# Kernel optimization log

Hardware: AMD Instinct MI355X
Metric: run time of the kernel (lower is better)

The kernel has to match this reference:

```python
import jax, jax.numpy as jnp
import numpy as np

MAX_LEN = 2048
D_MODEL = 1024
NUM_HEADS = 16
D_HEAD = D_MODEL // NUM_HEADS
BATCH = 2
SEQ = 2048


def setup_inputs() -> dict:
    key = jax.random.key(0)
    ks = jax.random.split(key, 8)
    scale = 1.0 / np.sqrt(D_MODEL)
    return {
        "x": jax.random.normal(ks[0], (BATCH, SEQ, D_MODEL), dtype=jnp.float32),
        "Wq": jax.random.normal(ks[1], (D_MODEL, D_MODEL), dtype=jnp.float32) * scale,
        "bq": jnp.zeros((D_MODEL,), dtype=jnp.float32),
        "Wk": jax.random.normal(ks[2], (D_MODEL, D_MODEL), dtype=jnp.float32) * scale,
        "bk": jnp.zeros((D_MODEL,), dtype=jnp.float32),
        "Wv": jax.random.normal(ks[3], (D_MODEL, D_MODEL), dtype=jnp.float32) * scale,
        "bv": jnp.zeros((D_MODEL,), dtype=jnp.float32),
        "Er": jax.random.normal(ks[4], (MAX_LEN, D_HEAD), dtype=jnp.float32),
    }


def _skew(QEr):
    # QEr: [B, H, S, S] -> Transformer-XL skew -> Srel: [B, H, S, S]
    B, H, S, _ = QEr.shape
    padded = jnp.pad(QEr, ((0, 0), (0, 0), (0, 0), (1, 0)))  # [B,H,S,S+1]
    reshaped = padded.reshape(B, H, S + 1, S)
    return reshaped[:, :, 1:, :]


def reference(x, Wq, bq, Wk, bk, Wv, bv, Er):
    B, S, D = x.shape
    H, dh = NUM_HEADS, D // NUM_HEADS
    q = (x @ Wq + bq).reshape(B, S, H, dh).transpose(0, 2, 1, 3)  # [B,H,S,dh]
    k = (x @ Wk + bk).reshape(B, S, H, dh).transpose(0, 2, 1, 3)
    v = (x @ Wv + bv).reshape(B, S, H, dh).transpose(0, 2, 1, 3)
    Er_s = Er[MAX_LEN - S:, :]                                    # [S, dh]
    QEr = jnp.einsum("bhsd,ld->bhsl", q, Er_s)                    # [B,H,S,S]
    Srel = _skew(QEr)
    QKt = jnp.einsum("bhsd,bhtd->bhst", q, k)
    attn = (QKt + Srel) / jnp.sqrt(jnp.asarray(dh, x.dtype))
    causal = jnp.tril(jnp.ones((S, S), dtype=bool))
    attn = jnp.where(causal[None, None], attn, -jnp.inf)
    attn = jax.nn.softmax(attn, axis=-1)
    out = jnp.einsum("bhst,bhtd->bhsd", attn, v)                  # [B,H,S,dh]
    return out.transpose(0, 2, 1, 3).reshape(B, S, D)             # dropout in eval = identity
```

## Files before the change

### kernel.cpp

```cpp
#include <hip/hip_runtime.h>
#include <hip/hip_bf16.h>

#define SLEN   2048
#define DMODEL 1024
#define NHEADS 16
#define DHEAD  64
#define NBATCH 2
#define EPAD_ROWS 2432

#define QSCALE 0.18033688011112042f
#define EXPB   23.083120654223414f

typedef __bf16 bf16x8 __attribute__((ext_vector_type(8)));
typedef float  f32x4  __attribute__((ext_vector_type(4)));

__device__ __forceinline__ unsigned short f2bf(float f) {
    unsigned int u = __builtin_bit_cast(unsigned int, f);
    return (unsigned short)((u + 0x7fffu + ((u >> 16) & 1u)) >> 16);
}

__device__ __forceinline__ float exp2_hw(float x) {
    float r;
    asm("v_exp_f32 %0, %1" : "=v"(r) : "v"(x));
    return r;
}

__device__ __forceinline__ unsigned int cvtpk_bf16(float lo, float hi) {
    unsigned int d;
    asm("v_cvt_pk_bf16_f32 %0, %1, %2" : "=v"(d) : "v"(lo), "v"(hi));
    return d;
}

__device__ __forceinline__ bf16x8 ld8(const unsigned short* p) {
    union { uint4 u; bf16x8 b; } t;
    t.u = *(const uint4*)p;
    return t.b;
}

__device__ __forceinline__ void glds16(const unsigned short* g, unsigned short* l) {
    __builtin_amdgcn_global_load_lds(
        (const __attribute__((address_space(1))) unsigned int*)g,
        (__attribute__((address_space(3))) unsigned int*)l, 16, 0, 0);
}

__global__ __launch_bounds__(256) void prep_kernel(
    const float* __restrict__ x, const float* __restrict__ Er,
    const float* __restrict__ Wq, const float* __restrict__ Wk,
    const float* __restrict__ Wv,
    unsigned short* __restrict__ xb, unsigned short* __restrict__ Ep,
    unsigned short* __restrict__ Wt) {
    const int bi = blockIdx.x, tid = threadIdx.x;
    if (bi < 4096) {
        int i = (bi * 256 + tid) * 4;
        float4 v = *(const float4*)(x + i);
        ushort4 o;
        o.x = f2bf(v.x); o.y = f2bf(v.y); o.z = f2bf(v.z); o.w = f2bf(v.w);
        *(ushort4*)(xb + i) = o;
    } else if (bi < 4704) {
        int i = (bi - 4096) * 256 + tid;
        int row = i >> 6;
        unsigned short v = 0;
        if (row < SLEN) v = f2bf(Er[i]);
        Ep[i] = v;
    } else {
        __shared__ float tile[32][33];
        const int b3 = bi - 4704;
        const int z = b3 >> 10, rem = b3 & 1023;
        const int n0 = (rem & 31) * 32, k0 = (rem >> 5) * 32;
        const float* W = (z == 0) ? Wq : (z == 1 ? Wk : Wv);
        unsigned short* out = Wt + (size_t)z * DMODEL * DMODEL;
        const int tx = tid & 31, ty = tid >> 5;
        for (int r = 0; r < 32; r += 8)
            tile[ty + r][tx] = W[(size_t)(k0 + ty + r) * DMODEL + n0 + tx];
        __syncthreads();
        for (int r = 0; r < 32; r += 8)
            out[(size_t)(n0 + ty + r) * DMODEL + k0 + tx] = f2bf(tile[tx][ty + r]);
    }
}

__global__ __launch_bounds__(256, 3) void qkv_gemm(
    const unsigned short* __restrict__ xb, const unsigned short* __restrict__ Wt,
    const float* __restrict__ bq, const float* __restrict__ bk, const float* __restrict__ bv,
    unsigned short* __restrict__ Qs, unsigned short* __restrict__ Ks,
    unsigned short* __restrict__ Vts) {
    const int b = blockIdx.x;
    const int x7 = b & 7, s = b >> 3;
    const int mt = ((x7 >> 1) << 3) | (s & 7);
    const int ntile = ((x7 & 1) << 2) | ((s >> 3) & 3);
    const int z = s >> 5;
    const int m0 = mt * 128, n0 = ntile * 128;

    const float* bias = (z == 0) ? bq : (z == 1 ? bk : bv);
    const unsigned short* Wz = Wt + (size_t)z * DMODEL * DMODEL;

    __shared__ __align__(16) unsigned short As[128][64];
    __shared__ __align__(16) unsigned short Bs[128][64];

    const int tid = threadIdx.x;
    const int wave = tid >> 6, lane = tid & 63, l16 = lane & 15, quad = lane >> 4;
    const int wm = (wave >> 1) * 64, wn = (wave & 1) * 64;

    const int lr8 = lane >> 3;
    const int sc  = ((lane & 7) ^ lr8) * 8;

    f32x4 acc[4][4];
#pragma unroll
    for (int mi = 0; mi < 4; mi++)
#pragma unroll
        for (int ni = 0; ni < 4; ni++) acc[mi][ni] = (f32x4){0.f, 0.f, 0.f, 0.f};

    for (int j = 0; j < 16; ++j) {
        if (j) __syncthreads();
        const int k0 = j * 64;
#pragma unroll
        for (int c = 0; c < 4; c++) {
            const int seg = wave * 4 + c;
            const int r8  = seg * 8 + lr8;
            glds16(&xb[(size_t)(m0 + r8) * DMODEL + k0 + sc], &As[seg * 8][0]);
            glds16(&Wz[(size_t)(n0 + r8) * DMODEL + k0 + sc], &Bs[seg * 8][0]);
        }
        __syncthreads();

        const unsigned short (*Aarr)[64] = (z == 2) ? Bs : As;
        const unsigned short (*Barr)[64] = (z == 2) ? As : Bs;
#pragma unroll
        for (int ks = 0; ks < 2; ks++) {
            const int pc = ((ks * 4 + quad) ^ (l16 & 7)) * 8;
            bf16x8 a[4], bb[4];
#pragma unroll
            for (int mi = 0; mi < 4; mi++) a[mi] = ld8(&Aarr[wm + mi * 16 + l16][pc]);
#pragma unroll
            for (int ni = 0; ni < 4; ni++) bb[ni] = ld8(&Barr[wn + ni * 16 + l16][pc]);
#pragma unroll
            for (int mi = 0; mi < 4; mi++)
#pragma unroll
                for (int ni = 0; ni < 4; ni++)
                    acc[mi][ni] = __builtin_amdgcn_mfma_f32_16x16x32_bf16(a[mi], bb[ni], acc[mi][ni], 0, 0, 0);
        }
    }

    if (z == 2) {
#pragma unroll
        for (int mi = 0; mi < 4; mi++)
#pragma unroll
            for (int r = 0; r < 4; r++) {
                const int n = n0 + wm + mi * 16 + quad * 4 + r;
                const float bb = bias[n];
                const int h = n >> 6, d = n & 63;
#pragma unroll
                for (int ni = 0; ni < 4; ni++) {
                    const int m = m0 + wn + ni * 16 + l16;
                    const int bi = m >> 11, ss = m & 2047;
                    Vts[((size_t)((bi * NHEADS + h) * 64 + d)) * SLEN + ss] = f2bf(acc[mi][ni][r] + bb);
                }
            }
    } else {
#pragma unroll
        for (int ni = 0; ni < 4; ni++) {
            const int n = n0 + wn + ni * 16 + l16;
            const float bb = bias[n];
            const int h = n >> 6, d = n & 63;
#pragma unroll
            for (int mi = 0; mi < 4; mi++)
#pragma unroll
                for (int r = 0; r < 4; r++) {
                    const int m = m0 + wm + mi * 16 + quad * 4 + r;
                    const int bi = m >> 11, ss = m & 2047;
                    float v = acc[mi][ni][r] + bb;
                    if (z == 0)
                        Qs[((size_t)(bi * NHEADS + h) * SLEN + ss) * 64 + d] = f2bf(v * QSCALE);
                    else
                        Ks[((size_t)(bi * NHEADS + h) * SLEN + ss) * 64 + d] = f2bf(v);
                }
        }
    }
}

__global__ __launch_bounds__(256, 2) void attn_kernel(
    const unsigned short* __restrict__ Q,
    const unsigned short* __restrict__ K,
    const unsigned short* __restrict__ Vt,
    const unsigned short* __restrict__ Ep,
    float* __restrict__ out) {
    const int tid = threadIdx.x;
    const int wave = tid >> 6, lane = tid & 63, l16 = lane & 15, quad = lane >> 4;
    const int lr8 = lane >> 3;
    const int swz = ((lane & 7) ^ lr8) * 8;

    const int bh = blockIdx.x & 31;
    const int pg = blockIdx.x >> 5;

    __shared__ __align__(16) unsigned short Ksh[2][64 * 64];
    __shared__ __align__(16) unsigned short Vsh[2][64 * 64];
    __shared__ __align__(16) unsigned short Esh[256 * 64];

    const unsigned short* Qb = Q + (size_t)bh * SLEN * 64;
    const unsigned short* Kb = K + (size_t)bh * SLEN * 64;
    const unsigned short* Vb = Vt + (size_t)bh * 64 * SLEN;
    const int ob = bh >> 4, oh = bh & 15;

    const int pc0 = (quad ^ (l16 & 7)) * 8;
    const int pc1 = ((4 + quad) ^ (l16 & 7)) * 8;
    const int krot = (15 - l16) & 3;
    const bool c1 = (krot & 1) != 0, c2 = (krot & 2) != 0;
    int permE[4]; bool hiE[4];
#pragma unroll
    for (int r = 0; r < 4; r++) {
        const int idx = quad * 4 + r + 15 - l16;
        permE[r] = ((idx >> 2) & 3) * 16 + l16;
        const int c  = r + 15 - l16;
        const int qv = (quad - (c >> 2)) & 3;
        hiE[r] = (qv * 4 + c) >= 16;
    }

    int s0 = pg * 64;
    int ntp = pg + 1;

#pragma unroll 1
    for (int pass = 0; pass < 2; ++pass) {
        const int sw = s0 + 16 * wave;
        const bf16x8 aq0 = ld8(Qb + (size_t)(sw + l16) * 64 + quad * 8);
        const bf16x8 aq1 = ld8(Qb + (size_t)(sw + l16) * 64 + 32 + quad * 8);

        f32x4 accO[4];
        float sacc[4];
#pragma unroll
        for (int nt = 0; nt < 4; nt++) accO[nt] = (f32x4){0.f, 0.f, 0.f, 0.f};
#pragma unroll
        for (int r = 0; r < 4; r++) sacc[r] = 0.f;

        const int p0row = SLEN - 64 - s0;

#pragma unroll
        for (int c = 0; c < 2; c++) {
            const int seg = wave * 2 + c;
            glds16(&Kb[(size_t)(seg * 8 + lr8) * 64 + swz], &Ksh[0][seg * 8 * 64]);
            glds16(&Vb[(size_t)(seg * 8 + lr8) * SLEN + swz], &Vsh[0][seg * 8 * 64]);
        }
#pragma unroll
        for (int u = 0; u < 6; u++) {
            const int idx = wave * 6 + u;
            const int grow = p0row + idx * 8;
            glds16(&Ep[(size_t)(grow + lr8) * 64 + swz], &Esh[(grow & 255) * 64]);
        }
        __syncthreads();

        for (int j = 0; j < ntp; ++j) {
            const int t0 = j * 64;
            const int cur = j & 1;

            if (j + 1 < ntp) {
                const int t1 = t0 + 64, nb = cur ^ 1;
#pragma unroll
                for (int c = 0; c < 2; c++) {
                    const int seg = wave * 2 + c;
                    glds16(&Kb[(size_t)(t1 + seg * 8 + lr8) * 64 + swz], &Ksh[nb][seg * 8 * 64]);
                    glds16(&Vb[(size_t)(seg * 8 + lr8) * SLEN + t1 + swz], &Vsh[nb][seg * 8 * 64]);
                }
                const int er = p0row + t0 + 128;
#pragma unroll
                for (int c = 0; c < 2; c++) {
                    const int seg = wave * 2 + c;
                    glds16(&Ep[(size_t)(er + seg * 8 + lr8) * 64 + swz],
                           &Esh[((er + seg * 8) & 255) * 64]);
                }
            }

            f32x4 accS[4];
#pragma unroll
            for (int nt = 0; nt < 4; nt++)
                accS[nt] = (f32x4){-EXPB, -EXPB, -EXPB, -EXPB};
#pragma unroll
            for (int nt = 0; nt < 4; nt++) {
                bf16x8 bk0 = ld8(&Ksh[cur][(nt * 16 + l16) * 64 + pc0]);
                bf16x8 bk1 = ld8(&Ksh[cur][(nt * 16 + l16) * 64 + pc1]);
                accS[nt] = __builtin_amdgcn_mfma_f32_16x16x32_bf16(bk0, aq0, accS[nt], 0, 0, 0);
                accS[nt] = __builtin_amdgcn_mfma_f32_16x16x32_bf16(bk1, aq1, accS[nt], 0, 0, 0);
            }

            const int rm0 = (SLEN - 16 - sw + t0) & 255;
            f32x4 accE[5];
#pragma unroll
            for (int nt = 0; nt < 5; nt++) accE[nt] = (f32x4){0.f, 0.f, 0.f, 0.f};
#pragma unroll
            for (int nt = 0; nt < 5; nt++) {
                const int rowm = (rm0 + nt * 16 + l16) & 255;
                bf16x8 be0 = ld8(&Esh[rowm * 64 + pc0]);
                bf16x8 be1 = ld8(&Esh[rowm * 64 + pc1]);
                accE[nt] = __builtin_amdgcn_mfma_f32_16x16x32_bf16(be0, aq0, accE[nt], 0, 0, 0);
                accE[nt] = __builtin_amdgcn_mfma_f32_16x16x32_bf16(be1, aq1, accE[nt], 0, 0, 0);
            }

            f32x4 rotE[5];
#pragma unroll
            for (int g = 0; g < 5; g++) {
                f32x4 A = accE[g], t, rt;
#pragma unroll
                for (int r = 0; r < 4; r++) t[r] = c1 ? A[(r + 1) & 3] : A[r];
#pragma unroll
                for (int r = 0; r < 4; r++) rt[r] = c2 ? t[(r + 2) & 3] : t[r];
                rotE[g] = rt;
            }

            float pe[4][4];
            auto scoreblk = [&](bool masked) {
#pragma unroll
                for (int nt = 0; nt < 4; nt++) {
#pragma unroll
                    for (int r = 0; r < 4; r++) {
                        float send = hiE[r] ? rotE[nt + 1][r] : rotE[nt][r];
                        float rel = __shfl(send, permE[r]);
                        float p = exp2_hw(accS[nt][r] + rel);
                        if (masked)
                            p = (t0 + nt * 16 + quad * 4 + r <= sw + l16) ? p : 0.0f;
                        sacc[r] += p;
                        pe[nt][r] = p;
                    }
                }
            };
            if (t0 + 63 <= sw) scoreblk(false);
            else               scoreblk(true);

            unsigned int w[4][2];
#pragma unroll
            for (int nt = 0; nt < 4; nt++) {
                w[nt][0] = cvtpk_bf16(pe[nt][0], pe[nt][1]);
                w[nt][1] = cvtpk_bf16(pe[nt][2], pe[nt][3]);
            }
            bf16x8 pf[2];
#pragma unroll
            for (int c = 0; c < 2; c++) {
                unsigned int a0 = w[2 * c][0], b0 = w[2 * c + 1][0];
                unsigned int a1 = w[2 * c][1], b1 = w[2 * c + 1][1];
                asm volatile("v_permlane32_swap_b32 %0, %1" : "+v"(a0), "+v"(b0));
                asm volatile("v_permlane16_swap_b32 %0, %1" : "+v"(a0), "+v"(b0));
                asm volatile("v_permlane32_swap_b32 %0, %1" : "+v"(a1), "+v"(b1));
                asm volatile("v_permlane16_swap_b32 %0, %1" : "+v"(a1), "+v"(b1));
                union { uint4 u; bf16x8 b; } t;
                t.u = (uint4){a0, a1, b0, b1};
                pf[c] = t.b;
            }

#pragma unroll
            for (int ntd = 0; ntd < 4; ntd++) {
                bf16x8 bv0 = ld8(&Vsh[cur][(ntd * 16 + l16) * 64 + pc0]);
                bf16x8 bv1 = ld8(&Vsh[cur][(ntd * 16 + l16) * 64 + pc1]);
                accO[ntd] = __builtin_amdgcn_mfma_f32_16x16x32_bf16(bv0, pf[0], accO[ntd], 0, 0, 0);
                accO[ntd] = __builtin_amdgcn_mfma_f32_16x16x32_bf16(bv1, pf[1], accO[ntd], 0, 0, 0);
            }

            __syncthreads();
        }

        float s4 = (sacc[0] + sacc[1]) + (sacc[2] + sacc[3]);
        s4 += __shfl_xor(s4, 16);
        s4 += __shfl_xor(s4, 32);
        const float inv = 1.f / s4;
        const int srow = sw + l16;
        float* orow = out + ((size_t)(ob * SLEN + srow)) * DMODEL + oh * 64 + quad * 4;
#pragma unroll
        for (int ntd = 0; ntd < 4; ntd++) {
            float4 st = {accO[ntd][0] * inv, accO[ntd][1] * inv,
                         accO[ntd][2] * inv, accO[ntd][3] * inv};
            *(float4*)(orow + ntd * 16) = st;
        }

        s0 = (31 - pg) * 64;
        ntp = 32 - pg;
    }
}

extern "C" void kernel_launch(void* const* d_in, const int* in_sizes, int n_in,
                              void* d_out, int out_size, void* d_ws, size_t ws_size,
                              hipStream_t stream) {
    const float* x  = (const float*)d_in[0];
    const float* Wq = (const float*)d_in[1];
    const float* bq = (const float*)d_in[2];
    const float* Wk = (const float*)d_in[3];
    const float* bk = (const float*)d_in[4];
    const float* Wv = (const float*)d_in[5];
    const float* bv = (const float*)d_in[6];
    const float* Er = (const float*)d_in[7];
    float* out = (float*)d_out;

    char* p = (char*)d_ws;
    unsigned short* xb  = (unsigned short*)p; p += (size_t)4096 * 1024 * 2;
    unsigned short* Wt  = (unsigned short*)p; p += (size_t)3 * 1024 * 1024 * 2;
    unsigned short* Qs  = (unsigned short*)p; p += (size_t)32 * 2048 * 64 * 2;
    unsigned short* Ks  = (unsigned short*)p; p += (size_t)32 * 2048 * 64 * 2;
    unsigned short* Vts = (unsigned short*)p; p += (size_t)32 * 2048 * 64 * 2;
    unsigned short* Ep  = (unsigned short*)p; p += (size_t)EPAD_ROWS * 64 * 2;

    hipLaunchKernelGGL(prep_kernel, dim3(7776), dim3(256), 0, stream,
                       x, Er, Wq, Wk, Wv, xb, Ep, Wt);
    hipLaunchKernelGGL(qkv_gemm, dim3(768), dim3(256), 0, stream,
                       xb, Wt, bq, bk, bv, Qs, Ks, Vts);
    hipLaunchKernelGGL(attn_kernel, dim3(512), dim3(256), 0, stream, Qs, Ks, Vts, Ep, out);
}
```

Baseline: 176.3 us.

## Stream Er rows from global into registers and drop the LDS ring buffer

Removes the 256-row shared-memory ring buffer for the relative-position embedding. Each lane now loads its Er fragments directly from global memory with inline global_load_dwordx4, and a manual vmcnt wait is placed before the QEr MFMAs. This cuts shared-memory use roughly in half, so the launch bounds are raised to allow three blocks per CU and the LDS staging traffic for Er goes away. In exchange it relies on hand-tuned waitcnt counting outside the compiler's knowledge. The K/V prefetch guard is also dropped, so the final iteration issues prefetch loads past the last tile, which may read beyond the buffer.

```diff
diff --git a/kernel.cpp b/kernel.cpp
--- a/kernel.cpp
+++ b/kernel.cpp
@@ -36,6 +36,16 @@
     t.u = *(const uint4*)p;
     return t.b;
 }
+
+__device__ __forceinline__ bf16x8 u2b(uint4 u) {
+    union { uint4 u; bf16x8 b; } t;
+    t.u = u;
+    return t.b;
+}
+
+#define LDG16(dst, ptr, offbytes)                                        \
+    asm volatile("global_load_dwordx4 %0, %1, off offset:" #offbytes     \
+                 : "=v"(dst) : "v"(ptr))
 
 __device__ __forceinline__ void glds16(const unsigned short* g, unsigned short* l) {
     __builtin_amdgcn_global_load_lds(
@@ -176,7 +186,7 @@
     }
 }
 
-__global__ __launch_bounds__(256, 2) void attn_kernel(
+__global__ __launch_bounds__(256, 3) void attn_kernel(
     const unsigned short* __restrict__ Q,
     const unsigned short* __restrict__ K,
     const unsigned short* __restrict__ Vt,
@@ -192,7 +202,6 @@
 
     __shared__ __align__(16) unsigned short Ksh[2][64 * 64];
     __shared__ __align__(16) unsigned short Vsh[2][64 * 64];
-    __shared__ __align__(16) unsigned short Esh[256 * 64];
 
     const unsigned short* Qb = Q + (size_t)bh * SLEN * 64;
     const unsigned short* Kb = K + (size_t)bh * SLEN * 64;
@@ -213,6 +222,8 @@
         hiE[r] = (qv * 4 + c) >= 16;
     }
 
+    const unsigned short* ep_lane = Ep + (size_t)l16 * 64 + quad * 8;
+
     int s0 = pg * 64;
     int ntp = pg + 1;
 
@@ -229,7 +240,7 @@
 #pragma unroll
         for (int r = 0; r < 4; r++) sacc[r] = 0.f;
 
-        const int p0row = SLEN - 64 - s0;
+        const unsigned short* eb0 = ep_lane + (size_t)(SLEN - 16 - sw) * 64;
 
 #pragma unroll
         for (int c = 0; c < 2; c++) {
@@ -237,19 +248,23 @@
             glds16(&Kb[(size_t)(seg * 8 + lr8) * 64 + swz], &Ksh[0][seg * 8 * 64]);
             glds16(&Vb[(size_t)(seg * 8 + lr8) * SLEN + swz], &Vsh[0][seg * 8 * 64]);
         }
-#pragma unroll
-        for (int u = 0; u < 6; u++) {
-            const int idx = wave * 6 + u;
-            const int grow = p0row + idx * 8;
-            glds16(&Ep[(size_t)(grow + lr8) * 64 + swz], &Esh[(grow & 255) * 64]);
-        }
         __syncthreads();
 
         for (int j = 0; j < ntp; ++j) {
             const int t0 = j * 64;
             const int cur = j & 1;
 
-            if (j + 1 < ntp) {
+            const unsigned short* e0 = eb0 + (size_t)t0 * 64;
+            const unsigned short* e1 = e0 + 2048;
+            const unsigned short* e2 = e0 + 4096;
+            uint4 eb[5][2];
+            LDG16(eb[0][0], e0, 0);    LDG16(eb[0][1], e0, 64);
+            LDG16(eb[1][0], e0, 2048); LDG16(eb[1][1], e0, 2112);
+            LDG16(eb[2][0], e1, 0);    LDG16(eb[2][1], e1, 64);
+            LDG16(eb[3][0], e1, 2048); LDG16(eb[3][1], e1, 2112);
+            LDG16(eb[4][0], e2, 0);    LDG16(eb[4][1], e2, 64);
+
+            {
                 const int t1 = t0 + 64, nb = cur ^ 1;
 #pragma unroll
                 for (int c = 0; c < 2; c++) {
@@ -257,13 +272,6 @@
                     glds16(&Kb[(size_t)(t1 + seg * 8 + lr8) * 64 + swz], &Ksh[nb][seg * 8 * 64]);
                     glds16(&Vb[(size_t)(seg * 8 + lr8) * SLEN + t1 + swz], &Vsh[nb][seg * 8 * 64]);
                 }
-                const int er = p0row + t0 + 128;
-#pragma unroll
-                for (int c = 0; c < 2; c++) {
-                    const int seg = wave * 2 + c;
-                    glds16(&Ep[(size_t)(er + seg * 8 + lr8) * 64 + swz],
-                           &Esh[((er + seg * 8) & 255) * 64]);
-                }
             }
 
             f32x4 accS[4];
@@ -278,17 +286,16 @@
                 accS[nt] = __builtin_amdgcn_mfma_f32_16x16x32_bf16(bk1, aq1, accS[nt], 0, 0, 0);
             }
 
-            const int rm0 = (SLEN - 16 - sw + t0) & 255;
+            asm volatile("s_waitcnt vmcnt(4)" ::: "memory");
+            __builtin_amdgcn_sched_barrier(0);
+
             f32x4 accE[5];
 #pragma unroll
             for (int nt = 0; nt < 5; nt++) accE[nt] = (f32x4){0.f, 0.f, 0.f, 0.f};
 #pragma unroll
             for (int nt = 0; nt < 5; nt++) {
-                const int rowm = (rm0 + nt * 16 + l16) & 255;
-                bf16x8 be0 = ld8(&Esh[rowm * 64 + pc0]);
-                bf16x8 be1 = ld8(&Esh[rowm * 64 + pc1]);
-                accE[nt] = __builtin_amdgcn_mfma_f32_16x16x32_bf16(be0, aq0, accE[nt], 0, 0, 0);
-                accE[nt] = __builtin_amdgcn_mfma_f32_16x16x32_bf16(be1, aq1, accE[nt], 0, 0, 0);
+                accE[nt] = __builtin_amdgcn_mfma_f32_16x16x32_bf16(u2b(eb[nt][0]), aq0, accE[nt], 0, 0, 0);
+                accE[nt] = __builtin_amdgcn_mfma_f32_16x16x32_bf16(u2b(eb[nt][1]), aq1, accE[nt], 0, 0, 0);
             }
 
             f32x4 rotE[5];
```

Result: slower. 209.4 us (+18.8%).

## Fuse Q/K/V projections per tile and reuse overlapping Er products

Applied to the files above, without the earlier changes.

The QKV GEMM now computes Q, K and V together for each 128x64 output tile. The x tile is loaded once and shared across all three weight matrices, which cuts A-operand global traffic and reduces the grid from 768 to 512 blocks, with occupancy dropped to 2 blocks per SM. In the attention kernel, the last QEr accumulator group of each key tile is carried into the first group of the next tile, which skips one redundant pair of MFMAs and LDS loads per iteration. The trade-off is more accumulator registers, lower occupancy and fewer blocks for load balancing in the GEMM.

```diff
diff --git a/kernel.cpp b/kernel.cpp
--- a/kernel.cpp
+++ b/kernel.cpp
@@ -78,36 +78,34 @@
     }
 }
 
-__global__ __launch_bounds__(256, 3) void qkv_gemm(
+__global__ __launch_bounds__(256, 2) void qkv_gemm(
     const unsigned short* __restrict__ xb, const unsigned short* __restrict__ Wt,
     const float* __restrict__ bq, const float* __restrict__ bk, const float* __restrict__ bv,
     unsigned short* __restrict__ Qs, unsigned short* __restrict__ Ks,
     unsigned short* __restrict__ Vts) {
     const int b = blockIdx.x;
-    const int x7 = b & 7, s = b >> 3;
-    const int mt = ((x7 >> 1) << 3) | (s & 7);
-    const int ntile = ((x7 & 1) << 2) | ((s >> 3) & 3);
-    const int z = s >> 5;
-    const int m0 = mt * 128, n0 = ntile * 128;
-
-    const float* bias = (z == 0) ? bq : (z == 1 ? bk : bv);
-    const unsigned short* Wz = Wt + (size_t)z * DMODEL * DMODEL;
+    const int mt = b & 31, nt = b >> 5;
+    const int m0 = mt * 128, n0 = nt * 64;
 
     __shared__ __align__(16) unsigned short As[128][64];
-    __shared__ __align__(16) unsigned short Bs[128][64];
+    __shared__ __align__(16) unsigned short Bs[3][64][64];
 
     const int tid = threadIdx.x;
     const int wave = tid >> 6, lane = tid & 63, l16 = lane & 15, quad = lane >> 4;
-    const int wm = (wave >> 1) * 64, wn = (wave & 1) * 64;
+    const int wm = (wave >> 1) * 64, wn2 = (wave & 1) * 32;
 
     const int lr8 = lane >> 3;
     const int sc  = ((lane & 7) ^ lr8) * 8;
 
-    f32x4 acc[4][4];
+    f32x4 accQ[4][2], accK[4][2], accV[2][4];
 #pragma unroll
     for (int mi = 0; mi < 4; mi++)
 #pragma unroll
-        for (int ni = 0; ni < 4; ni++) acc[mi][ni] = (f32x4){0.f, 0.f, 0.f, 0.f};
+        for (int ni = 0; ni < 2; ni++) {
+            accQ[mi][ni] = (f32x4){0.f, 0.f, 0.f, 0.f};
+            accK[mi][ni] = (f32x4){0.f, 0.f, 0.f, 0.f};
+            accV[ni][mi] = (f32x4){0.f, 0.f, 0.f, 0.f};
+        }
 
     for (int j = 0; j < 16; ++j) {
         if (j) __syncthreads();
@@ -115,65 +113,72 @@
 #pragma unroll
         for (int c = 0; c < 4; c++) {
             const int seg = wave * 4 + c;
-            const int r8  = seg * 8 + lr8;
-            glds16(&xb[(size_t)(m0 + r8) * DMODEL + k0 + sc], &As[seg * 8][0]);
-            glds16(&Wz[(size_t)(n0 + r8) * DMODEL + k0 + sc], &Bs[seg * 8][0]);
+            glds16(&xb[(size_t)(m0 + seg * 8 + lr8) * DMODEL + k0 + sc], &As[seg * 8][0]);
+        }
+#pragma unroll
+        for (int c = 0; c < 6; c++) {
+            const int idx = wave * 6 + c;
+            const int z = idx >> 3, seg = idx & 7;
+            glds16(&Wt[(size_t)z * DMODEL * DMODEL + (size_t)(n0 + seg * 8 + lr8) * DMODEL + k0 + sc],
+                   &Bs[z][seg * 8][0]);
         }
         __syncthreads();
 
-        const unsigned short (*Aarr)[64] = (z == 2) ? Bs : As;
-        const unsigned short (*Barr)[64] = (z == 2) ? As : Bs;
 #pragma unroll
         for (int ks = 0; ks < 2; ks++) {
             const int pc = ((ks * 4 + quad) ^ (l16 & 7)) * 8;
-            bf16x8 a[4], bb[4];
-#pragma unroll
-            for (int mi = 0; mi < 4; mi++) a[mi] = ld8(&Aarr[wm + mi * 16 + l16][pc]);
-#pragma unroll
-            for (int ni = 0; ni < 4; ni++) bb[ni] = ld8(&Barr[wn + ni * 16 + l16][pc]);
+            bf16x8 a[4], bb[3][2];
+#pragma unroll
+            for (int mi = 0; mi < 4; mi++) a[mi] = ld8(&As[wm + mi * 16 + l16][pc]);
+#pragma unroll
+            for (int z = 0; z < 3; z++)
+#pragma unroll
+                for (int ni = 0; ni < 2; ni++) bb[z][ni] = ld8(&Bs[z][wn2 + ni * 16 + l16][pc]);
 #pragma unroll
             for (int mi = 0; mi < 4; mi++)
 #pragma unroll
-                for (int ni = 0; ni < 4; ni++)
-                    acc[mi][ni] = __builtin_amdgcn_mfma_f32_16x16x32_bf16(a[mi], bb[ni], acc[mi][ni], 0, 0, 0);
+                for (int ni = 0; ni < 2; ni++) {
+                    accQ[mi][ni] = __builtin_amdgcn_mfma_f32_16x16x32_bf16(a[mi], bb[0][ni], accQ[mi][ni], 0, 0, 0);
+                    accK[mi][ni] = __builtin_amdgcn_mfma_f32_16x16x32_bf16(a[mi], bb[1][ni], accK[mi][ni], 0, 0, 0);
+                    accV[ni][mi] = __builtin_amdgcn_mfma_f32_16x16x32_bf16(bb[2][ni], a[mi], accV[ni][mi], 0, 0, 0);
+                }
         }
     }
 
-    if (z == 2) {
+    const int hh = n0 >> 6;
+
+#pragma unroll
+    for (int ni = 0; ni < 2; ni++) {
+        const int n = n0 + wn2 + ni * 16 + l16;
+        const float bqv = bq[n], bkv = bk[n];
+        const int d = n & 63;
 #pragma unroll
         for (int mi = 0; mi < 4; mi++)
 #pragma unroll
             for (int r = 0; r < 4; r++) {
-                const int n = n0 + wm + mi * 16 + quad * 4 + r;
-                const float bb = bias[n];
-                const int h = n >> 6, d = n & 63;
-#pragma unroll
-                for (int ni = 0; ni < 4; ni++) {
-                    const int m = m0 + wn + ni * 16 + l16;
-                    const int bi = m >> 11, ss = m & 2047;
-                    Vts[((size_t)((bi * NHEADS + h) * 64 + d)) * SLEN + ss] = f2bf(acc[mi][ni][r] + bb);
-                }
-            }
-    } else {
-#pragma unroll
-        for (int ni = 0; ni < 4; ni++) {
-            const int n = n0 + wn + ni * 16 + l16;
-            const float bb = bias[n];
-            const int h = n >> 6, d = n & 63;
-#pragma unroll
-            for (int mi = 0; mi < 4; mi++)
-#pragma unroll
-                for (int r = 0; r < 4; r++) {
-                    const int m = m0 + wm + mi * 16 + quad * 4 + r;
-                    const int bi = m >> 11, ss = m & 2047;
-                    float v = acc[mi][ni][r] + bb;
-                    if (z == 0)
-                        Qs[((size_t)(bi * NHEADS + h) * SLEN + ss) * 64 + d] = f2bf(v * QSCALE);
-                    else
-                        Ks[((size_t)(bi * NHEADS + h) * SLEN + ss) * 64 + d] = f2bf(v);
-                }
-        }
+                const int m = m0 + wm + mi * 16 + quad * 4 + r;
+                const int bi = m >> 11, s = m & 2047;
+                Qs[((size_t)(bi * NHEADS + hh) * SLEN + s) * 64 + d] =
+                    f2bf((accQ[mi][ni][r] + bqv) * QSCALE);
+                Ks[((size_t)(bi * NHEADS + hh) * SLEN + s) * 64 + d] =
+                    f2bf(accK[mi][ni][r] + bkv);
+            }
     }
+#pragma unroll
+    for (int ni = 0; ni < 2; ni++)
+#pragma unroll
+        for (int r = 0; r < 4; r++) {
+            const int n = n0 + wn2 + ni * 16 + quad * 4 + r;
+            const float bvv = bv[n];
+            const int d = n & 63;
+#pragma unroll
+            for (int mi = 0; mi < 4; mi++) {
+                const int m = m0 + wm + mi * 16 + l16;
+                const int bi = m >> 11, s = m & 2047;
+                Vts[((size_t)((bi * NHEADS + hh) * 64 + d)) * SLEN + s] =
+                    f2bf(accV[ni][mi][r] + bvv);
+            }
+        }
 }
 
 __global__ __launch_bounds__(256, 2) void attn_kernel(
@@ -245,6 +250,8 @@
         }
         __syncthreads();
 
+        f32x4 carryE = (f32x4){0.f, 0.f, 0.f, 0.f};
+
         for (int j = 0; j < ntp; ++j) {
             const int t0 = j * 64;
             const int cur = j & 1;
@@ -280,16 +287,26 @@
 
             const int rm0 = (SLEN - 16 - sw + t0) & 255;
             f32x4 accE[5];
-#pragma unroll
-            for (int nt = 0; nt < 5; nt++) accE[nt] = (f32x4){0.f, 0.f, 0.f, 0.f};
-#pragma unroll
-            for (int nt = 0; nt < 5; nt++) {
+            if (j == 0) {
+                accE[0] = (f32x4){0.f, 0.f, 0.f, 0.f};
+                const int rowm = (rm0 + l16) & 255;
+                bf16x8 be0 = ld8(&Esh[rowm * 64 + pc0]);
+                bf16x8 be1 = ld8(&Esh[rowm * 64 + pc1]);
+                accE[0] = __builtin_amdgcn_mfma_f32_16x16x32_bf16(be0, aq0, accE[0], 0, 0, 0);
+                accE[0] = __builtin_amdgcn_mfma_f32_16x16x32_bf16(be1, aq1, accE[0], 0, 0, 0);
+            } else {
+                accE[0] = carryE;
+            }
+#pragma unroll
+            for (int nt = 1; nt < 5; nt++) {
+                accE[nt] = (f32x4){0.f, 0.f, 0.f, 0.f};
                 const int rowm = (rm0 + nt * 16 + l16) & 255;
                 bf16x8 be0 = ld8(&Esh[rowm * 64 + pc0]);
                 bf16x8 be1 = ld8(&Esh[rowm * 64 + pc1]);
                 accE[nt] = __builtin_amdgcn_mfma_f32_16x16x32_bf16(be0, aq0, accE[nt], 0, 0, 0);
                 accE[nt] = __builtin_amdgcn_mfma_f32_16x16x32_bf16(be1, aq1, accE[nt], 0, 0, 0);
             }
+            carryE = accE[4];
 
             f32x4 rotE[5];
 #pragma unroll
@@ -393,7 +410,7 @@
 
     hipLaunchKernelGGL(prep_kernel, dim3(7776), dim3(256), 0, stream,
                        x, Er, Wq, Wk, Wv, xb, Ep, Wt);
-    hipLaunchKernelGGL(qkv_gemm, dim3(768), dim3(256), 0, stream,
+    hipLaunchKernelGGL(qkv_gemm, dim3(512), dim3(256), 0, stream,
                        xb, Wt, bq, bk, bv, Qs, Ks, Vts);
     hipLaunchKernelGGL(attn_kernel, dim3(512), dim3(256), 0, stream, Qs, Ks, Vts, Ep, out);
 }
```

New measurement: 171.1 us. 3.0% less time.
